# Kernel tuning notes

Measured on AMD Instinct MI355X. Metric: run time of the kernel, lower is better.

Reference implementation:

```python
import jax, jax.numpy as jnp
import numpy as np

EPS = 1e-5

def _layer_norm(x, gamma, beta):
    mu = jnp.mean(x, axis=-1, keepdims=True)
    var = jnp.mean(jnp.square(x - mu), axis=-1, keepdims=True)
    return (x - mu) * jax.lax.rsqrt(var + EPS) * gamma + beta

def setup_inputs() -> dict:
    key = jax.random.key(0)
    ks = jax.random.split(key, 16)
    B, N, E, D = 1024, 64, 1024, 512
    s_e = 1.0 / np.sqrt(E)
    s_d = 1.0 / np.sqrt(D)
    return {
        "role_embeddings": jax.random.normal(ks[0], (B, N, E), jnp.float32),
        "context": jax.random.normal(ks[1], (B, D), jnp.float32),
        "qW": jax.random.uniform(ks[2], (E, E), jnp.float32, -s_e, s_e),
        "qb": jax.random.uniform(ks[3], (E,), jnp.float32, -s_e, s_e),
        "kW": jax.random.uniform(ks[4], (E, D), jnp.float32, -s_d, s_d),
        "kb": jax.random.uniform(ks[5], (E,), jnp.float32, -s_d, s_d),
        "vW": jax.random.uniform(ks[6], (E, D), jnp.float32, -s_d, s_d),
        "vb": jax.random.uniform(ks[7], (E,), jnp.float32, -s_d, s_d),
        "oW": jax.random.uniform(ks[8], (E, E), jnp.float32, -s_e, s_e),
        "ob": jax.random.uniform(ks[9], (E,), jnp.float32, -s_e, s_e),
        "lnq_g": jnp.ones((E,), jnp.float32),
        "lnq_b": jnp.zeros((E,), jnp.float32),
        "lnk_g": jnp.ones((D,), jnp.float32),
        "lnk_b": jnp.zeros((D,), jnp.float32),
    }

def reference(role_embeddings, context, qW, qb, kW, kb, vW, vb, oW, ob, lnq_g, lnq_b, lnk_g, lnk_b):
    E = role_embeddings.shape[-1]
    ctx = context[:, None, :]                                   # [B, 1, D]
    q = _layer_norm(role_embeddings, lnq_g, lnq_b) @ qW.T + qb  # [B, N, E]
    nk = _layer_norm(ctx, lnk_g, lnk_b)                         # [B, 1, D]
    k = nk @ kW.T + kb                                          # [B, 1, E]
    v = nk @ vW.T + vb                                          # [B, 1, E]
    scale = E ** (-0.5)
    scores = jnp.einsum('bne,bke->bnk', q, k) * scale           # [B, N, 1]
    attn = jnp.tanh(scores)
    out = attn * v                                              # broadcast -> [B, N, E]
    return (out + role_embeddings) @ oW.T + ob
```

## Files before the change

kernel.cpp:

```cpp
#include <hip/hip_runtime.h>

#define E_DIM 1024
#define D_DIM 512
#define B_DIM 1024
#define N_SEQ 64
#define M_ROWS (B_DIM * N_SEQ)

typedef __attribute__((ext_vector_type(8))) short bf16x8;
typedef __attribute__((ext_vector_type(4))) float f32x4;
typedef __attribute__((ext_vector_type(8))) unsigned short u16x8;
typedef __attribute__((ext_vector_type(4))) unsigned short u16x4;

__device__ __forceinline__ float bf2f(unsigned short b) {
    union { unsigned int u; float f; } v; v.u = ((unsigned int)b) << 16; return v.f;
}
__device__ __forceinline__ unsigned short f2bf(float f) {
    union { float f; unsigned int u; } v; v.f = f;
    unsigned int r = v.u + 0x7FFFu + ((v.u >> 16) & 1u);
    return (unsigned short)(r >> 16);
}
__device__ __forceinline__ bool detect_bf16(const void* det) {
    return *(const unsigned int*)det == 0x3F803F80u;
}
__device__ __forceinline__ void load8(const void* p, size_t idx, bool isbf, float o[8]) {
    if (isbf) {
        const u16x8 v = *(const u16x8*)((const unsigned short*)p + idx);
#pragma unroll
        for (int j = 0; j < 8; j++) o[j] = bf2f(v[j]);
    } else {
        const float4 a = *(const float4*)((const float*)p + idx);
        const float4 b = *(const float4*)((const float*)p + idx + 4);
        o[0]=a.x; o[1]=a.y; o[2]=a.z; o[3]=a.w; o[4]=b.x; o[5]=b.y; o[6]=b.z; o[7]=b.w;
    }
}
__device__ __forceinline__ float load1(const void* p, size_t idx, bool isbf) {
    return isbf ? bf2f(((const unsigned short*)p)[idx]) : ((const float*)p)[idx];
}
__device__ __forceinline__ void gload16(const void* g, void* l) {
    __builtin_amdgcn_global_load_lds((const __attribute__((address_space(1))) void*)g,
                                     (__attribute__((address_space(3))) void*)l, 16, 0, 0);
}

__device__ __forceinline__ void block_reduce_2(float& s, float& s2, float* smem) {
#pragma unroll
    for (int off = 32; off; off >>= 1) {
        s  += __shfl_xor(s,  off, 64);
        s2 += __shfl_xor(s2, off, 64);
    }
    const int wave = threadIdx.x >> 6, lane = threadIdx.x & 63;
    if (lane == 0) { smem[wave * 2] = s; smem[wave * 2 + 1] = s2; }
    __syncthreads();
    s  = smem[0] + smem[2] + smem[4] + smem[6];
    s2 = smem[1] + smem[3] + smem[5] + smem[7];
}
__device__ __forceinline__ void block_reduce_3(float& a, float& b, float& c, float* smem) {
#pragma unroll
    for (int off = 32; off; off >>= 1) {
        a += __shfl_xor(a, off, 64);
        b += __shfl_xor(b, off, 64);
        c += __shfl_xor(c, off, 64);
    }
    const int wave = threadIdx.x >> 6, lane = threadIdx.x & 63;
    if (lane == 0) { smem[wave * 3] = a; smem[wave * 3 + 1] = b; smem[wave * 3 + 2] = c; }
    __syncthreads();
    a = smem[0] + smem[3] + smem[6] + smem[9];
    b = smem[1] + smem[4] + smem[7] + smem[10];
    c = smem[2] + smem[5] + smem[8] + smem[11];
}

__global__ void ctxln_k(const void* __restrict__ ctx, const void* __restrict__ g,
                        const void* __restrict__ bta, const void* __restrict__ det,
                        float* __restrict__ nk) {
    __shared__ float sm[8];
    const bool isbf = detect_bf16(det);
    const size_t base = (size_t)blockIdx.x * D_DIM;
    const int t = threadIdx.x;
    const float x0 = load1(ctx, base + t * 2, isbf);
    const float x1 = load1(ctx, base + t * 2 + 1, isbf);
    float s = x0 + x1, s2 = x0 * x0 + x1 * x1;
    block_reduce_2(s, s2, sm);
    const float m = s * (1.f / D_DIM);
    const float rs = rsqrtf(s2 * (1.f / D_DIM) - m * m + 1e-5f);
    nk[base + t * 2]     = (x0 - m) * rs * load1(g, t * 2, isbf)     + load1(bta, t * 2, isbf);
    nk[base + t * 2 + 1] = (x1 - m) * rs * load1(g, t * 2 + 1, isbf) + load1(bta, t * 2 + 1, isbf);
}

__global__ void transpose_k(const void* __restrict__ Win, const void* __restrict__ det,
                            float* __restrict__ out) {
    __shared__ float tile[32][33];
    const bool isbf = detect_bf16(det);
    const int bx = blockIdx.x * 32, by = blockIdx.y * 32;
    const int tx = threadIdx.x & 31, ty4 = (threadIdx.x >> 5) * 4;
#pragma unroll
    for (int i = 0; i < 4; i++)
        tile[ty4 + i][tx] = load1(Win, (size_t)(by + ty4 + i) * E_DIM + bx + tx, isbf);
    __syncthreads();
#pragma unroll
    for (int i = 0; i < 4; i++)
        out[(size_t)(bx + ty4 + i) * E_DIM + by + tx] = tile[tx][ty4 + i];
}

__global__ void castw_k(const void* __restrict__ Win, const void* __restrict__ det,
                        unsigned short* __restrict__ out, int n) {
    const bool isbf = detect_bf16(det);
    const int i = (blockIdx.x * 256 + threadIdx.x) * 8;
    if (i >= n) return;
    float a8[8];
    load8(Win, (size_t)i, isbf, a8);
    u16x8 h;
#pragma unroll
    for (int j = 0; j < 8; j++) h[j] = f2bf(a8[j]);
    *(u16x8*)(out + i) = h;
}

template <int KDIM>
__launch_bounds__(256)
__global__ void sgemm2_k(const float* __restrict__ A0, const void* __restrict__ W0,
                         const void* __restrict__ b0, float* __restrict__ C0_,
                         const float* __restrict__ A1, const void* __restrict__ W1,
                         const void* __restrict__ b1, float* __restrict__ C1_,
                         const void* __restrict__ det, int w0f32, int w1f32) {
    __shared__ __align__(16) unsigned short As[64][40];
    __shared__ __align__(16) unsigned short Bs[64][40];
    const bool sel = blockIdx.x >= 16;
    const float* A = sel ? A1 : A0;
    const void* W = sel ? W1 : W0;
    const void* bias = sel ? b1 : b0;
    float* C = sel ? C1_ : C0_;
    const bool wbf = (sel ? w1f32 : w0f32) ? false : detect_bf16(det);
    const int tid = threadIdx.x;
    const int tileM = blockIdx.y * 64;
    const int tileN = (blockIdx.x & 15) * 64;
    const int r = tid >> 2;
    const int cseg = (tid & 3) * 8;
    const int gm = tileM + r;
    const int gn = tileN + r;
    const int lane = tid & 63;
    const int wave = tid >> 6;
    const int quad = lane >> 4;
    const int l16 = lane & 15;

    f32x4 acc[4];
#pragma unroll
    for (int i = 0; i < 4; i++) acc[i] = (f32x4){0.f, 0.f, 0.f, 0.f};

    for (int k0 = 0; k0 < KDIM; k0 += 32) {
        const int gk = k0 + cseg;
        float a8[8], w8[8];
        load8(A, (size_t)gm * KDIM + gk, false, a8);
        load8(W, (size_t)gn * KDIM + gk, wbf, w8);
        __syncthreads();
#pragma unroll
        for (int j = 0; j < 8; j++) {
            As[r][cseg + j] = f2bf(a8[j]);
            Bs[r][cseg + j] = f2bf(w8[j]);
        }
        __syncthreads();
        const bf16x8 a = *(const bf16x8*)&As[wave * 16 + l16][quad * 8];
#pragma unroll
        for (int nt = 0; nt < 4; nt++) {
            const bf16x8 b = *(const bf16x8*)&Bs[nt * 16 + l16][quad * 8];
            acc[nt] = __builtin_amdgcn_mfma_f32_16x16x32_bf16(a, b, acc[nt], 0, 0, 0);
        }
    }
#pragma unroll
    for (int nt = 0; nt < 4; nt++) {
        const int gc = tileN + nt * 16 + l16;
        const float bv = bias ? load1(bias, gc, detect_bf16(det)) : 0.f;
#pragma unroll
        for (int rg = 0; rg < 4; rg++) {
            const int grow = tileM + wave * 16 + quad * 4 + rg;
            C[(size_t)grow * E_DIM + gc] = acc[nt][rg] + bv;
        }
    }
}

__global__ void prep_k(const float* __restrict__ kvec, float* __restrict__ kkgk,
                       const void* __restrict__ qb, const void* __restrict__ g,
                       const void* __restrict__ bta, const void* __restrict__ det,
                       float* __restrict__ S1, float* __restrict__ C0) {
    __shared__ float sm[12];
    const bool isbf = detect_bf16(det);
    const size_t base = (size_t)blockIdx.x * E_DIM;
    const int t = threadIdx.x;
    float c = 0.f, s1 = 0.f, s2 = 0.f;
#pragma unroll
    for (int j = 0; j < 4; j++) {
        const int idx = t * 4 + j;
        const float kv = kvec[base + idx], kkv = kkgk[base + idx];
        const float gv = load1(g, idx, isbf);
        c  += load1(qb, idx, isbf) * kv;
        s1 += gv * kkv;
        s2 += load1(bta, idx, isbf) * kkv;
        kkgk[base + idx] = gv * kkv;
    }
    block_reduce_3(c, s1, s2, sm);
    if (t == 0) { S1[blockIdx.x] = s1; C0[blockIdx.x] = s2 + c; }
}

__global__ void rowscore_k(const void* __restrict__ role, const void* __restrict__ det,
                           const float* __restrict__ gk, const float* __restrict__ S1,
                           const float* __restrict__ C0, float* __restrict__ attn,
                           unsigned short* __restrict__ roleb) {
    const bool isbf = detect_bf16(det);
    const int lane = threadIdx.x & 63;
    const int gw = blockIdx.x * 4 + (threadIdx.x >> 6);
    const int nw = gridDim.x * 4;
    const bool wb = (!isbf) && (roleb != nullptr);
    for (int m = gw; m < M_ROWS; m += nw) {
        const int b = m >> 6;
        const size_t base = (size_t)m * E_DIM;
        const float* gkb = gk + ((size_t)b << 10);
        float s = 0.f, s2 = 0.f, d = 0.f;
        if (isbf) {
            const unsigned short* rp = (const unsigned short*)role + base;
#pragma unroll
            for (int j = 0; j < 2; j++) {
                const int col = lane * 8 + j * 512;
                const u16x8 v = *(const u16x8*)(rp + col);
                const float4 g0 = *(const float4*)(gkb + col);
                const float4 g1 = *(const float4*)(gkb + col + 4);
                float x[8];
#pragma unroll
                for (int i = 0; i < 8; i++) x[i] = bf2f(v[i]);
#pragma unroll
                for (int i = 0; i < 8; i++) { s += x[i]; s2 += x[i] * x[i]; }
                d += x[0]*g0.x + x[1]*g0.y + x[2]*g0.z + x[3]*g0.w
                   + x[4]*g1.x + x[5]*g1.y + x[6]*g1.z + x[7]*g1.w;
            }
        } else {
            const float* rp = (const float*)role + base;
#pragma unroll
            for (int j = 0; j < 4; j++) {
                const int col = lane * 4 + j * 256;
                const float4 x = *(const float4*)(rp + col);
                const float4 g = *(const float4*)(gkb + col);
                s  += x.x + x.y + x.z + x.w;
                s2 += x.x*x.x + x.y*x.y + x.z*x.z + x.w*x.w;
                d  += x.x*g.x + x.y*g.y + x.z*g.z + x.w*g.w;
                if (wb) {
                    u16x4 h; h[0]=f2bf(x.x); h[1]=f2bf(x.y); h[2]=f2bf(x.z); h[3]=f2bf(x.w);
                    *(u16x4*)(roleb + base + col) = h;
                }
            }
        }
#pragma unroll
        for (int off = 32; off; off >>= 1) {
            s  += __shfl_xor(s,  off, 64);
            s2 += __shfl_xor(s2, off, 64);
            d  += __shfl_xor(d,  off, 64);
        }
        if (lane == 0) {
            const float mu = s * (1.f / E_DIM);
            const float rstd = rsqrtf(s2 * (1.f / E_DIM) - mu * mu + 1e-5f);
            attn[m] = tanhf((rstd * (d - mu * S1[b]) + C0[b]) * 0.03125f);
        }
    }
}

__launch_bounds__(256)
__global__ void outgemm_k(const void* __restrict__ role, const unsigned short* __restrict__ roleb,
                          const unsigned short* __restrict__ oWb,
                          const float* __restrict__ attn, const float* __restrict__ vo,
                          const void* __restrict__ ob, void* __restrict__ out,
                          const void* __restrict__ det) {
    __shared__ __align__(16) unsigned short As[128 * 32];
    __shared__ __align__(16) unsigned short Bs[128 * 32];
    const bool isbf = detect_bf16(det);
    const bool abf = isbf || (roleb != nullptr);
    const unsigned short* Ab = isbf ? (const unsigned short*)role : roleb;
    const int tid = threadIdx.x;
    const int wave = tid >> 6, lane = tid & 63;
    const int quad = lane >> 4, l16 = lane & 15;
    const int wm = wave >> 1, wn = wave & 1;

    const int id = blockIdx.x + (blockIdx.y << 3);
    const int sid = (id & 7) * 512 + (id >> 3);
    const int tileN = (sid & 7) * 128;
    const int tileM = (sid >> 3) * 128;

    const int srow = lane >> 2;
    const int scol = (lane & 3) * 8;
    const int ar = tid >> 2;
    const int ac = (tid & 3) * 8;

    f32x4 acc[4][4];
#pragma unroll
    for (int i = 0; i < 4; i++)
#pragma unroll
        for (int j = 0; j < 4; j++) acc[i][j] = (f32x4){0.f, 0.f, 0.f, 0.f};

    const float* rolef = (const float*)role;

    for (int k0 = 0; k0 < E_DIM; k0 += 32) {
        __syncthreads();
#pragma unroll
        for (int c = 0; c < 2; c++) {
            const int cb = c * 4 + wave;
            const unsigned short* gp = oWb + (size_t)(tileN + cb * 16 + srow) * E_DIM + k0 + scol;
            gload16(gp, Bs + cb * 512);
        }
        if (abf) {
#pragma unroll
            for (int c = 0; c < 2; c++) {
                const int cb = c * 4 + wave;
                const unsigned short* gp = Ab + (size_t)(tileM + cb * 16 + srow) * E_DIM + k0 + scol;
                gload16(gp, As + cb * 512);
            }
        } else {
#pragma unroll
            for (int c = 0; c < 2; c++) {
                const int rr = c * 64 + ar;
                const float* gp = rolef + (size_t)(tileM + rr) * E_DIM + k0 + ac;
                const float4 f0 = ((const float4*)gp)[0];
                const float4 f1 = ((const float4*)gp)[1];
                u16x8 h;
                h[0]=f2bf(f0.x); h[1]=f2bf(f0.y); h[2]=f2bf(f0.z); h[3]=f2bf(f0.w);
                h[4]=f2bf(f1.x); h[5]=f2bf(f1.y); h[6]=f2bf(f1.z); h[7]=f2bf(f1.w);
                *(u16x8*)(As + rr * 32 + ac) = h;
            }
        }
        __syncthreads();
        bf16x8 af[4], bfr[4];
#pragma unroll
        for (int mt = 0; mt < 4; mt++)
            af[mt] = *(const bf16x8*)(As + (wm * 64 + mt * 16 + l16) * 32 + quad * 8);
#pragma unroll
        for (int nt = 0; nt < 4; nt++)
            bfr[nt] = *(const bf16x8*)(Bs + (wn * 64 + nt * 16 + l16) * 32 + quad * 8);
#pragma unroll
        for (int mt = 0; mt < 4; mt++)
#pragma unroll
            for (int nt = 0; nt < 4; nt++)
                acc[mt][nt] = __builtin_amdgcn_mfma_f32_16x16x32_bf16(af[mt], bfr[nt], acc[mt][nt], 0, 0, 0);
    }
    const int b = (tileM >> 6) + wm;
    float at[4][4];
#pragma unroll
    for (int mt = 0; mt < 4; mt++)
#pragma unroll
        for (int rg = 0; rg < 4; rg++)
            at[mt][rg] = attn[tileM + wm * 64 + mt * 16 + quad * 4 + rg];
#pragma unroll
    for (int nt = 0; nt < 4; nt++) {
        const int gc = tileN + wn * 64 + nt * 16 + l16;
        const float bv = load1(ob, gc, isbf);
        const float vv = vo[((size_t)b << 10) + gc];
#pragma unroll
        for (int mt = 0; mt < 4; mt++) {
#pragma unroll
            for (int rg = 0; rg < 4; rg++) {
                const int grow = tileM + wm * 64 + mt * 16 + quad * 4 + rg;
                const float val = acc[mt][nt][rg] + at[mt][rg] * vv + bv;
                const size_t off = (size_t)grow * E_DIM + gc;
                if (isbf) ((unsigned short*)out)[off] = f2bf(val);
                else      ((float*)out)[off] = val;
            }
        }
    }
}

extern "C" void kernel_launch(void* const* d_in, const int* in_sizes, int n_in,
                              void* d_out, int out_size, void* d_ws, size_t ws_size,
                              hipStream_t stream) {
    const void* role  = d_in[0];
    const void* ctx   = d_in[1];
    const void* qW    = d_in[2];
    const void* qb    = d_in[3];
    const void* kW    = d_in[4];
    const void* kb    = d_in[5];
    const void* vW    = d_in[6];
    const void* vb    = d_in[7];
    const void* oW    = d_in[8];
    const void* ob    = d_in[9];
    const void* lnq_g = d_in[10];
    const void* lnq_b = d_in[11];
    const void* lnk_g = d_in[12];
    const void* lnk_b = d_in[13];

    float* ws    = (float*)d_ws;
    float* kvec  = ws;
    float* vvec  = kvec + (1 << 20);
    float* slotA = vvec + (1 << 20);
    float* kkgk  = slotA + (1 << 20);
    float* vo    = kkgk + (1 << 20);
    float* attn  = vo + (1 << 20);
    float* S1    = attn + (1 << 16);
    float* C0    = S1 + 1024;
    float* wend  = C0 + 1024;
    const size_t used = (size_t)(wend - ws) * 4;
    unsigned short* roleb = nullptr;
    if (ws_size >= used + (size_t)M_ROWS * E_DIM * 2)
        roleb = (unsigned short*)wend;

    float* nk = slotA;
    ctxln_k<<<B_DIM, 256, 0, stream>>>(ctx, lnk_g, lnk_b, lnq_g, nk);
    sgemm2_k<D_DIM><<<dim3(32, 16), 256, 0, stream>>>(
        nk, kW, kb, kvec, nk, vW, vb, vvec, lnq_g, 0, 0);
    float* qWT = slotA;
    transpose_k<<<dim3(32, 32), 256, 0, stream>>>(qW, lnq_g, qWT);
    sgemm2_k<E_DIM><<<dim3(32, 16), 256, 0, stream>>>(
        kvec, qWT, nullptr, kkgk, vvec, oW, nullptr, vo, lnq_g, 1, 0);
    prep_k<<<B_DIM, 256, 0, stream>>>(kvec, kkgk, qb, lnq_g, lnq_b, lnq_g, S1, C0);
    unsigned short* oWb = (unsigned short*)slotA;
    castw_k<<<512, 256, 0, stream>>>(oW, lnq_g, oWb, E_DIM * E_DIM);
    rowscore_k<<<2048, 256, 0, stream>>>(role, lnq_g, kkgk, S1, C0, attn, roleb);
    outgemm_k<<<dim3(8, 512), 256, 0, stream>>>(role, roleb, oWb, attn, vo, ob, d_out, lnq_g);
}
```

Measured before the change: 804.0 us.

## Double-buffer LDS in output GEMM and merge prep kernels into one launch

```diff
diff --git a/kernel.cpp b/kernel.cpp
--- a/kernel.cpp
+++ b/kernel.cpp
@@ -68,49 +68,47 @@
     c = smem[2] + smem[5] + smem[8] + smem[11];
 }
 
-__global__ void ctxln_k(const void* __restrict__ ctx, const void* __restrict__ g,
-                        const void* __restrict__ bta, const void* __restrict__ det,
-                        float* __restrict__ nk) {
-    __shared__ float sm[8];
+__global__ void prep1_k(const void* __restrict__ ctx, const void* __restrict__ g,
+                        const void* __restrict__ bta, const void* __restrict__ qW,
+                        const void* __restrict__ oW, const void* __restrict__ det,
+                        float* __restrict__ nk, float* __restrict__ qWT,
+                        unsigned short* __restrict__ oWb) {
     const bool isbf = detect_bf16(det);
-    const size_t base = (size_t)blockIdx.x * D_DIM;
+    const int bid = blockIdx.x;
     const int t = threadIdx.x;
-    const float x0 = load1(ctx, base + t * 2, isbf);
-    const float x1 = load1(ctx, base + t * 2 + 1, isbf);
-    float s = x0 + x1, s2 = x0 * x0 + x1 * x1;
-    block_reduce_2(s, s2, sm);
-    const float m = s * (1.f / D_DIM);
-    const float rs = rsqrtf(s2 * (1.f / D_DIM) - m * m + 1e-5f);
-    nk[base + t * 2]     = (x0 - m) * rs * load1(g, t * 2, isbf)     + load1(bta, t * 2, isbf);
-    nk[base + t * 2 + 1] = (x1 - m) * rs * load1(g, t * 2 + 1, isbf) + load1(bta, t * 2 + 1, isbf);
-}
-
-__global__ void transpose_k(const void* __restrict__ Win, const void* __restrict__ det,
-                            float* __restrict__ out) {
-    __shared__ float tile[32][33];
-    const bool isbf = detect_bf16(det);
-    const int bx = blockIdx.x * 32, by = blockIdx.y * 32;
-    const int tx = threadIdx.x & 31, ty4 = (threadIdx.x >> 5) * 4;
-#pragma unroll
-    for (int i = 0; i < 4; i++)
-        tile[ty4 + i][tx] = load1(Win, (size_t)(by + ty4 + i) * E_DIM + bx + tx, isbf);
-    __syncthreads();
-#pragma unroll
-    for (int i = 0; i < 4; i++)
-        out[(size_t)(bx + ty4 + i) * E_DIM + by + tx] = tile[tx][ty4 + i];
-}
-
-__global__ void castw_k(const void* __restrict__ Win, const void* __restrict__ det,
-                        unsigned short* __restrict__ out, int n) {
-    const bool isbf = detect_bf16(det);
-    const int i = (blockIdx.x * 256 + threadIdx.x) * 8;
-    if (i >= n) return;
-    float a8[8];
-    load8(Win, (size_t)i, isbf, a8);
-    u16x8 h;
-#pragma unroll
-    for (int j = 0; j < 8; j++) h[j] = f2bf(a8[j]);
-    *(u16x8*)(out + i) = h;
+    if (bid < B_DIM) {
+        if (bid < 512) {
+            const int i = (bid * 256 + t) * 8;
+            float a8[8];
+            load8(oW, (size_t)i, isbf, a8);
+            u16x8 h;
+#pragma unroll
+            for (int j = 0; j < 8; j++) h[j] = f2bf(a8[j]);
+            *(u16x8*)(oWb + i) = h;
+        }
+        __shared__ float sm[8];
+        const size_t base = (size_t)bid * D_DIM;
+        const float x0 = load1(ctx, base + t * 2, isbf);
+        const float x1 = load1(ctx, base + t * 2 + 1, isbf);
+        float s = x0 + x1, s2 = x0 * x0 + x1 * x1;
+        block_reduce_2(s, s2, sm);
+        const float m = s * (1.f / D_DIM);
+        const float rs = rsqrtf(s2 * (1.f / D_DIM) - m * m + 1e-5f);
+        nk[base + t * 2]     = (x0 - m) * rs * load1(g, t * 2, isbf)     + load1(bta, t * 2, isbf);
+        nk[base + t * 2 + 1] = (x1 - m) * rs * load1(g, t * 2 + 1, isbf) + load1(bta, t * 2 + 1, isbf);
+    } else {
+        const int i = bid - B_DIM;
+        const int bx = (i & 31) * 32, by = (i >> 5) * 32;
+        __shared__ float tile[32][33];
+        const int tx = t & 31, ty4 = (t >> 5) * 4;
+#pragma unroll
+        for (int j = 0; j < 4; j++)
+            tile[ty4 + j][tx] = load1(qW, (size_t)(by + ty4 + j) * E_DIM + bx + tx, isbf);
+        __syncthreads();
+#pragma unroll
+        for (int j = 0; j < 4; j++)
+            qWT[(size_t)(bx + ty4 + j) * E_DIM + by + tx] = tile[tx][ty4 + j];
+    }
 }
 
 template <int KDIM>
@@ -264,11 +262,12 @@
                           const float* __restrict__ attn, const float* __restrict__ vo,
                           const void* __restrict__ ob, void* __restrict__ out,
                           const void* __restrict__ det) {
-    __shared__ __align__(16) unsigned short As[128 * 32];
-    __shared__ __align__(16) unsigned short Bs[128 * 32];
+    __shared__ __align__(16) unsigned short As[2][128 * 32];
+    __shared__ __align__(16) unsigned short Bs[2][128 * 32];
     const bool isbf = detect_bf16(det);
     const bool abf = isbf || (roleb != nullptr);
     const unsigned short* Ab = isbf ? (const unsigned short*)role : roleb;
+    const float* rolef = (const float*)role;
     const int tid = threadIdx.x;
     const int wave = tid >> 6, lane = tid & 63;
     const int quad = lane >> 4, l16 = lane & 15;
@@ -290,22 +289,19 @@
 #pragma unroll
         for (int j = 0; j < 4; j++) acc[i][j] = (f32x4){0.f, 0.f, 0.f, 0.f};
 
-    const float* rolef = (const float*)role;
-
-    for (int k0 = 0; k0 < E_DIM; k0 += 32) {
-        __syncthreads();
+    auto stage = [&](int buf, int k0) {
 #pragma unroll
         for (int c = 0; c < 2; c++) {
             const int cb = c * 4 + wave;
-            const unsigned short* gp = oWb + (size_t)(tileN + cb * 16 + srow) * E_DIM + k0 + scol;
-            gload16(gp, Bs + cb * 512);
+            gload16(oWb + (size_t)(tileN + cb * 16 + srow) * E_DIM + k0 + scol,
+                    &Bs[buf][cb * 512]);
         }
         if (abf) {
 #pragma unroll
             for (int c = 0; c < 2; c++) {
                 const int cb = c * 4 + wave;
-                const unsigned short* gp = Ab + (size_t)(tileM + cb * 16 + srow) * E_DIM + k0 + scol;
-                gload16(gp, As + cb * 512);
+                gload16(Ab + (size_t)(tileM + cb * 16 + srow) * E_DIM + k0 + scol,
+                        &As[buf][cb * 512]);
             }
         } else {
 #pragma unroll
@@ -317,23 +313,37 @@
                 u16x8 h;
                 h[0]=f2bf(f0.x); h[1]=f2bf(f0.y); h[2]=f2bf(f0.z); h[3]=f2bf(f0.w);
                 h[4]=f2bf(f1.x); h[5]=f2bf(f1.y); h[6]=f2bf(f1.z); h[7]=f2bf(f1.w);
-                *(u16x8*)(As + rr * 32 + ac) = h;
+                *(u16x8*)(&As[buf][rr * 32 + ac]) = h;
             }
         }
+    };
+    auto compute = [&](int buf) {
+        bf16x8 af[4], bfr[4];
+#pragma unroll
+        for (int mt = 0; mt < 4; mt++)
+            af[mt] = *(const bf16x8*)(&As[buf][(wm * 64 + mt * 16 + l16) * 32 + quad * 8]);
+#pragma unroll
+        for (int nt = 0; nt < 4; nt++)
+            bfr[nt] = *(const bf16x8*)(&Bs[buf][(wn * 64 + nt * 16 + l16) * 32 + quad * 8]);
+#pragma unroll
+        for (int mt = 0; mt < 4; mt++)
+#pragma unroll
+            for (int nt = 0; nt < 4; nt++)
+                acc[mt][nt] = __builtin_amdgcn_mfma_f32_16x16x32_bf16(af[mt], bfr[nt],
+                                                                      acc[mt][nt], 0, 0, 0);
+    };
+
+    stage(0, 0);
+    __syncthreads();
+    int cur = 0;
+    for (int t = 0; t < 31; ++t) {
+        stage(cur ^ 1, (t + 1) * 32);
+        compute(cur);
         __syncthreads();
-        bf16x8 af[4], bfr[4];
-#pragma unroll
-        for (int mt = 0; mt < 4; mt++)
-            af[mt] = *(const bf16x8*)(As + (wm * 64 + mt * 16 + l16) * 32 + quad * 8);
-#pragma unroll
-        for (int nt = 0; nt < 4; nt++)
-            bfr[nt] = *(const bf16x8*)(Bs + (wn * 64 + nt * 16 + l16) * 32 + quad * 8);
-#pragma unroll
-        for (int mt = 0; mt < 4; mt++)
-#pragma unroll
-            for (int nt = 0; nt < 4; nt++)
-                acc[mt][nt] = __builtin_amdgcn_mfma_f32_16x16x32_bf16(af[mt], bfr[nt], acc[mt][nt], 0, 0, 0);
-    }
+        cur ^= 1;
+    }
+    compute(cur);
+
     const int b = (tileM >> 6) + wm;
     float at[4][4];
 #pragma unroll
@@ -381,10 +391,12 @@
     float* ws    = (float*)d_ws;
     float* kvec  = ws;
     float* vvec  = kvec + (1 << 20);
-    float* slotA = vvec + (1 << 20);
-    float* kkgk  = slotA + (1 << 20);
+    float* nk    = vvec + (1 << 20);
+    float* qWT   = nk + (1 << 19);
+    float* kkgk  = qWT + (1 << 20);
     float* vo    = kkgk + (1 << 20);
-    float* attn  = vo + (1 << 20);
+    unsigned short* oWb = (unsigned short*)(vo + (1 << 20));
+    float* attn  = (float*)oWb + (1 << 19);
     float* S1    = attn + (1 << 16);
     float* C0    = S1 + 1024;
     float* wend  = C0 + 1024;
@@ -393,17 +405,12 @@
     if (ws_size >= used + (size_t)M_ROWS * E_DIM * 2)
         roleb = (unsigned short*)wend;
 
-    float* nk = slotA;
-    ctxln_k<<<B_DIM, 256, 0, stream>>>(ctx, lnk_g, lnk_b, lnq_g, nk);
+    prep1_k<<<2048, 256, 0, stream>>>(ctx, lnk_g, lnk_b, qW, oW, lnq_g, nk, qWT, oWb);
     sgemm2_k<D_DIM><<<dim3(32, 16), 256, 0, stream>>>(
         nk, kW, kb, kvec, nk, vW, vb, vvec, lnq_g, 0, 0);
-    float* qWT = slotA;
-    transpose_k<<<dim3(32, 32), 256, 0, stream>>>(qW, lnq_g, qWT);
     sgemm2_k<E_DIM><<<dim3(32, 16), 256, 0, stream>>>(
         kvec, qWT, nullptr, kkgk, vvec, oW, nullptr, vo, lnq_g, 1, 0);
     prep_k<<<B_DIM, 256, 0, stream>>>(kvec, kkgk, qb, lnq_g, lnq_b, lnq_g, S1, C0);
-    unsigned short* oWb = (unsigned short*)slotA;
-    castw_k<<<512, 256, 0, stream>>>(oW, lnq_g, oWb, E_DIM * E_DIM);
     rowscore_k<<<2048, 256, 0, stream>>>(role, lnq_g, kkgk, S1, C0, attn, roleb);
     outgemm_k<<<dim3(8, 512), 256, 0, stream>>>(role, roleb, oWb, attn, vo, ob, d_out, lnq_g);
 }
```

Measured after the change: 786.3 us. -2.2%, faster.
